# Performance work log

Hardware: AMD Instinct MI355X
Metric: run time of the kernel (lower is better)

## Reference

```python
import jax, jax.numpy as jnp
from jax import lax
import numpy as np

KERNEL_SIZE = 24

def setup_inputs() -> dict:
    key = jax.random.key(0)
    k1, k2, k3, k4 = jax.random.split(key, 4)
    B, C, T = 16, 1024, 3000
    x = jax.random.normal(k1, (B, C, T, 1), dtype=jnp.float32)
    alpha = jax.random.uniform(k2, (C,), dtype=jnp.float32)   # in (0,1): decaying kernels
    beta = jax.random.normal(k3, (C,), dtype=jnp.float32)
    theta = jax.random.uniform(k4, (C,), dtype=jnp.float32)
    return {"x": x, "alpha": alpha, "beta": beta, "theta": theta}

def _cos_approx(x):
    x2 = x * x
    return 1.0 - 0.5 * x2 + (x2 * x2) * (1.0 / 24.0)

def reference(x, alpha, beta, theta):
    B, C, T, _ = x.shape
    K = KERNEL_SIZE
    t_idx = jnp.arange(K, dtype=x.dtype)                      # (K,)
    log_alpha = jnp.log(jnp.clip(alpha, 1e-6))                # (C,)
    decay = jnp.exp(log_alpha[:, None] * t_idx)               # (C,K)
    phase = _cos_approx(theta[:, None] * t_idx)               # (C,K)
    kernel = (beta[:, None] * decay * phase)[:, None, :]      # (C,1,K) depthwise
    # causal depthwise conv1d: left-pad K-1 (torch F.conv1d and lax conv are both correlations)
    y = lax.conv_general_dilated(
        x[..., 0], kernel,
        window_strides=(1,), padding=[(K - 1, 0)],
        dimension_numbers=("NCH", "OIH", "NCH"),
        feature_group_count=C,
    )                                                         # (B,C,T)
    return y[..., None]                                       # (B,C,T,1)
```

## Files before the change

kernel.cpp:

```cpp
#include <hip/hip_runtime.h>


#define KSZ   24
#define T_LEN 3000
#define C_CH  1024
#define B_N   16
#define TPB   256
#define OPT   4
#define TILE  (TPB * OPT)
#define CHK   (T_LEN / 4)
#define PADC  (KSZ / 4)
#define LMAX  (CHK + PADC - 1)
#define PPOS(L) ((L) + ((L) >> 3))
#define LDSN  (PPOS(LMAX) + 1)

typedef float f32x4 __attribute__((ext_vector_type(4)));

__device__ __forceinline__ float cos_approx(float v) {
    float v2 = v * v;
    return 1.0f - 0.5f * v2 + (v2 * v2) * (1.0f / 24.0f);
}

__global__ __launch_bounds__(TPB) void ssm4d_conv(
        const float* __restrict__ x,
        const float* __restrict__ alpha,
        const float* __restrict__ beta,
        const float* __restrict__ theta,
        float* __restrict__ y) {
    const int row   = blockIdx.x;
    const int c     = row & (C_CH - 1);
    const long base = (long)row * T_LEN;
    const int tid   = threadIdx.x;

    __shared__ float ws[KSZ];
    __shared__ f32x4 lds[LDSN];

    const f32x4* xp = (const f32x4*)(x + base);
    const int c0 = tid, c1 = tid + TPB, c2 = tid + 2 * TPB;
    f32x4 a0 = xp[c0];
    f32x4 a1 = xp[c1];
    f32x4 a2 = (c2 < CHK) ? xp[c2] : (f32x4){0.f, 0.f, 0.f, 0.f};

    if (tid < KSZ) {
        const int k = (KSZ - 1) - tid;
        const float a   = fmaxf(alpha[c], 1e-6f);
        const float dec = expf(logf(a) * (float)k);
        ws[tid] = beta[c] * dec * cos_approx(theta[c] * (float)k);
    }
    if (tid < PADC) lds[tid] = (f32x4){0.f, 0.f, 0.f, 0.f};

    lds[PPOS(c0 + PADC)] = a0;
    lds[PPOS(c1 + PADC)] = a1;
    if (c2 < CHK) lds[PPOS(c2 + PADC)] = a2;
    __syncthreads();

    float wr[KSZ];
#pragma unroll
    for (int d = 0; d < KSZ; ++d) wr[d] = ws[d];

#pragma unroll
    for (int s = 0; s < 3; ++s) {
        const int t = s * TILE + tid * OPT;
        if (t < T_LEN) {
            float win[KSZ + OPT];
            const int L0 = s * (TILE / 4) + tid;
#pragma unroll
            for (int q = 0; q < (KSZ + OPT) / 4; ++q) {
                f32x4 v = lds[PPOS(L0 + q)];
                win[4 * q + 0] = v.x; win[4 * q + 1] = v.y;
                win[4 * q + 2] = v.z; win[4 * q + 3] = v.w;
            }
            float acc[OPT];
#pragma unroll
            for (int m = 0; m < OPT; ++m) acc[m] = 0.0f;
#pragma unroll
            for (int d = 0; d < KSZ; ++d) {
#pragma unroll
                for (int m = 0; m < OPT; ++m)
                    acc[m] = fmaf(wr[d], win[KSZ + m - d], acc[m]);
            }
            *(float4*)(y + base + t) = make_float4(acc[0], acc[1], acc[2], acc[3]);
        }
    }
}

extern "C" void kernel_launch(void* const* d_in, const int* in_sizes, int n_in,
                              void* d_out, int out_size, void* d_ws, size_t ws_size,
                              hipStream_t stream) {
    const float* x     = (const float*)d_in[0];
    const float* alpha = (const float*)d_in[1];
    const float* beta  = (const float*)d_in[2];
    const float* theta = (const float*)d_in[3];
    float* y = (float*)d_out;

    ssm4d_conv<<<B_N * C_CH, TPB, 0, stream>>>(x, alpha, beta, theta, y);
}
```

Before: 328.1 us.

## Process four rows per block with double-buffered async global-to-LDS loads

Each block now handles four consecutive rows instead of one. The next row's input is prefetched straight into a second LDS buffer with global_load_lds while the current row is convolved, and its filter taps are computed in the same step. This aims to hide global load latency and spread per-block launch and setup cost over more work. In exchange it drops the padded LDS indexing, which may bring back bank conflicts, and it relies on the barrier waiting for the async LDS loads to finish.

After: 337.4 us. +2.8%, slower.

```diff
diff --git a/kernel.cpp b/kernel.cpp
--- a/kernel.cpp
+++ b/kernel.cpp
@@ -10,9 +10,9 @@
 #define TILE  (TPB * OPT)
 #define CHK   (T_LEN / 4)
 #define PADC  (KSZ / 4)
-#define LMAX  (CHK + PADC - 1)
-#define PPOS(L) ((L) + ((L) >> 3))
-#define LDSN  (PPOS(LMAX) + 1)
+#define NCHK  (CHK + PADC)
+#define RPB   4
+#define NBLK  ((B_N * C_CH) / RPB)
 
 typedef float f32x4 __attribute__((ext_vector_type(4)));
 
@@ -21,66 +21,96 @@
     return 1.0f - 0.5f * v2 + (v2 * v2) * (1.0f / 24.0f);
 }
 
+__device__ __forceinline__ void gload16(const float* g, float* l) {
+    __builtin_amdgcn_global_load_lds(
+        (const __attribute__((address_space(1))) void*)g,
+        (__attribute__((address_space(3))) void*)l,
+        16, 0, 0);
+}
+
+__device__ __forceinline__ void stage_row(const float* xr, f32x4* buf, int tid) {
+    gload16(xr + tid * 4,             (float*)&buf[PADC + tid]);
+    gload16(xr + (tid + TPB) * 4,     (float*)&buf[PADC + TPB + tid]);
+    if (tid + 2 * TPB < CHK)
+        gload16(xr + (tid + 2 * TPB) * 4, (float*)&buf[PADC + 2 * TPB + tid]);
+}
+
+__device__ __forceinline__ void calc_w(const float* __restrict__ alpha,
+                                       const float* __restrict__ beta,
+                                       const float* __restrict__ theta,
+                                       int row, float* wsrow, int tid) {
+    if (tid < KSZ) {
+        const int c = row & (C_CH - 1);
+        const int k = (KSZ - 1) - tid;
+        const float a = fmaxf(alpha[c], 1e-6f);
+        wsrow[tid] = beta[c] * expf(logf(a) * (float)k)
+                   * cos_approx(theta[c] * (float)k);
+    }
+}
+
 __global__ __launch_bounds__(TPB) void ssm4d_conv(
         const float* __restrict__ x,
         const float* __restrict__ alpha,
         const float* __restrict__ beta,
         const float* __restrict__ theta,
         float* __restrict__ y) {
-    const int row   = blockIdx.x;
-    const int c     = row & (C_CH - 1);
-    const long base = (long)row * T_LEN;
-    const int tid   = threadIdx.x;
+    const int tid  = threadIdx.x;
+    const int row0 = blockIdx.x * RPB;
 
-    __shared__ float ws[KSZ];
-    __shared__ f32x4 lds[LDSN];
+    __shared__ f32x4 buf[2][NCHK];
+    __shared__ float ws[2][KSZ];
 
-    const f32x4* xp = (const f32x4*)(x + base);
-    const int c0 = tid, c1 = tid + TPB, c2 = tid + 2 * TPB;
-    f32x4 a0 = xp[c0];
-    f32x4 a1 = xp[c1];
-    f32x4 a2 = (c2 < CHK) ? xp[c2] : (f32x4){0.f, 0.f, 0.f, 0.f};
+    if (tid < PADC) {
+        buf[0][tid] = (f32x4){0.f, 0.f, 0.f, 0.f};
+        buf[1][tid] = (f32x4){0.f, 0.f, 0.f, 0.f};
+    }
 
-    if (tid < KSZ) {
-        const int k = (KSZ - 1) - tid;
-        const float a   = fmaxf(alpha[c], 1e-6f);
-        const float dec = expf(logf(a) * (float)k);
-        ws[tid] = beta[c] * dec * cos_approx(theta[c] * (float)k);
-    }
-    if (tid < PADC) lds[tid] = (f32x4){0.f, 0.f, 0.f, 0.f};
-
-    lds[PPOS(c0 + PADC)] = a0;
-    lds[PPOS(c1 + PADC)] = a1;
-    if (c2 < CHK) lds[PPOS(c2 + PADC)] = a2;
+    stage_row(x + (long)row0 * T_LEN, buf[0], tid);
+    calc_w(alpha, beta, theta, row0, ws[0], tid);
     __syncthreads();
 
-    float wr[KSZ];
+    int cur = 0;
+#pragma unroll 1
+    for (int r = 0; r < RPB; ++r) {
+        const int nxt = cur ^ 1;
+
+        if (r + 1 < RPB) {
+            stage_row(x + (long)(row0 + r + 1) * T_LEN, buf[nxt], tid);
+            calc_w(alpha, beta, theta, row0 + r + 1, ws[nxt], tid);
+        }
+
+        float wr[KSZ];
 #pragma unroll
-    for (int d = 0; d < KSZ; ++d) wr[d] = ws[d];
+        for (int d = 0; d < KSZ; ++d) wr[d] = ws[cur][d];
 
+        float* yr = y + (long)(row0 + r) * T_LEN;
 #pragma unroll
-    for (int s = 0; s < 3; ++s) {
-        const int t = s * TILE + tid * OPT;
-        if (t < T_LEN) {
-            float win[KSZ + OPT];
-            const int L0 = s * (TILE / 4) + tid;
+        for (int s = 0; s < 3; ++s) {
+            const int t = s * TILE + tid * OPT;
+            if (t < T_LEN) {
+                const int L0 = s * (TILE / 4) + tid;
+                float win[KSZ + OPT];
 #pragma unroll
-            for (int q = 0; q < (KSZ + OPT) / 4; ++q) {
-                f32x4 v = lds[PPOS(L0 + q)];
-                win[4 * q + 0] = v.x; win[4 * q + 1] = v.y;
-                win[4 * q + 2] = v.z; win[4 * q + 3] = v.w;
+                for (int q = 0; q < (KSZ + OPT) / 4; ++q) {
+                    f32x4 v = buf[cur][L0 + q];
+                    win[4 * q + 0] = v.x; win[4 * q + 1] = v.y;
+                    win[4 * q + 2] = v.z; win[4 * q + 3] = v.w;
+                }
+                float acc[OPT];
+#pragma unroll
+                for (int m = 0; m < OPT; ++m) acc[m] = 0.0f;
+#pragma unroll
+                for (int d = 0; d < KSZ; ++d) {
+#pragma unroll
+                    for (int m = 0; m < OPT; ++m)
+                        acc[m] = fmaf(wr[d], win[KSZ + m - d], acc[m]);
+                }
+                *(float4*)(yr + t) = make_float4(acc[0], acc[1], acc[2], acc[3]);
             }
-            float acc[OPT];
-#pragma unroll
-            for (int m = 0; m < OPT; ++m) acc[m] = 0.0f;
-#pragma unroll
-            for (int d = 0; d < KSZ; ++d) {
-#pragma unroll
-                for (int m = 0; m < OPT; ++m)
-                    acc[m] = fmaf(wr[d], win[KSZ + m - d], acc[m]);
-            }
-            *(float4*)(y + base + t) = make_float4(acc[0], acc[1], acc[2], acc[3]);
         }
+
+        __syncthreads();
+        cur = nxt;
     }
 }
 
@@ -93,5 +123,5 @@
     const float* theta = (const float*)d_in[3];
     float* y = (float*)d_out;
 
-    ssm4d_conv<<<B_N * C_CH, TPB, 0, stream>>>(x, alpha, beta, theta, y);
+    ssm4d_conv<<<NBLK, TPB, 0, stream>>>(x, alpha, beta, theta, y);
 }
```

## Load rows directly to LDS and compute 12 outputs per thread

Applied to the files above, without the earlier changes.

Global loads now go straight into LDS through the global_load_lds builtin, bypassing VGPRs, and the padded LDS indexing is removed. Each thread now computes 12 contiguous outputs instead of three passes of 4. Only 250 of 256 threads are active, which cuts the redundant window loads per output, and launch bounds now request 4 blocks per CU. The costs are LDS bank conflicts from the stride-3 f32x4 reads without padding and higher register pressure.

After: 336.6 us. 1.03x slower.

```diff
diff --git a/kernel.cpp b/kernel.cpp
--- a/kernel.cpp
+++ b/kernel.cpp
@@ -6,13 +6,12 @@
 #define C_CH  1024
 #define B_N   16
 #define TPB   256
-#define OPT   4
-#define TILE  (TPB * OPT)
+#define OPT   12
+#define ACT   (T_LEN / OPT)
 #define CHK   (T_LEN / 4)
 #define PADC  (KSZ / 4)
-#define LMAX  (CHK + PADC - 1)
-#define PPOS(L) ((L) + ((L) >> 3))
-#define LDSN  (PPOS(LMAX) + 1)
+#define NCHK  (CHK + PADC)
+#define WIN   (KSZ + OPT)
 
 typedef float f32x4 __attribute__((ext_vector_type(4)));
 
@@ -21,7 +20,14 @@
     return 1.0f - 0.5f * v2 + (v2 * v2) * (1.0f / 24.0f);
 }
 
-__global__ __launch_bounds__(TPB) void ssm4d_conv(
+__device__ __forceinline__ void gload16(const float* g, float* l) {
+    __builtin_amdgcn_global_load_lds(
+        (const __attribute__((address_space(1))) void*)g,
+        (__attribute__((address_space(3))) void*)l,
+        16, 0, 0);
+}
+
+__global__ __launch_bounds__(TPB, 4) void ssm4d_conv(
         const float* __restrict__ x,
         const float* __restrict__ alpha,
         const float* __restrict__ beta,
@@ -32,55 +38,54 @@
     const long base = (long)row * T_LEN;
     const int tid   = threadIdx.x;
 
+    __shared__ f32x4 buf[NCHK];
     __shared__ float ws[KSZ];
-    __shared__ f32x4 lds[LDSN];
 
-    const f32x4* xp = (const f32x4*)(x + base);
-    const int c0 = tid, c1 = tid + TPB, c2 = tid + 2 * TPB;
-    f32x4 a0 = xp[c0];
-    f32x4 a1 = xp[c1];
-    f32x4 a2 = (c2 < CHK) ? xp[c2] : (f32x4){0.f, 0.f, 0.f, 0.f};
+    const float* xr = x + base;
+    gload16(xr + tid * 4,             (float*)&buf[PADC + tid]);
+    gload16(xr + (tid + TPB) * 4,     (float*)&buf[PADC + TPB + tid]);
+    if (tid + 2 * TPB < CHK)
+        gload16(xr + (tid + 2 * TPB) * 4, (float*)&buf[PADC + 2 * TPB + tid]);
 
     if (tid < KSZ) {
         const int k = (KSZ - 1) - tid;
-        const float a   = fmaxf(alpha[c], 1e-6f);
-        const float dec = expf(logf(a) * (float)k);
-        ws[tid] = beta[c] * dec * cos_approx(theta[c] * (float)k);
+        const float a = fmaxf(alpha[c], 1e-6f);
+        ws[tid] = beta[c] * expf(logf(a) * (float)k)
+                * cos_approx(theta[c] * (float)k);
     }
-    if (tid < PADC) lds[tid] = (f32x4){0.f, 0.f, 0.f, 0.f};
+    if (tid < PADC) buf[tid] = (f32x4){0.f, 0.f, 0.f, 0.f};
 
-    lds[PPOS(c0 + PADC)] = a0;
-    lds[PPOS(c1 + PADC)] = a1;
-    if (c2 < CHK) lds[PPOS(c2 + PADC)] = a2;
     __syncthreads();
 
-    float wr[KSZ];
+    if (tid < ACT) {
+        float wr[KSZ];
 #pragma unroll
-    for (int d = 0; d < KSZ; ++d) wr[d] = ws[d];
+        for (int d = 0; d < KSZ; ++d) wr[d] = ws[d];
 
+        float win[WIN];
+        const f32x4* wp = &buf[3 * tid];
 #pragma unroll
-    for (int s = 0; s < 3; ++s) {
-        const int t = s * TILE + tid * OPT;
-        if (t < T_LEN) {
-            float win[KSZ + OPT];
-            const int L0 = s * (TILE / 4) + tid;
+        for (int q = 0; q < WIN / 4; ++q) {
+            f32x4 v = wp[q];
+            win[4 * q + 0] = v.x; win[4 * q + 1] = v.y;
+            win[4 * q + 2] = v.z; win[4 * q + 3] = v.w;
+        }
+
+        float acc[OPT];
 #pragma unroll
-            for (int q = 0; q < (KSZ + OPT) / 4; ++q) {
-                f32x4 v = lds[PPOS(L0 + q)];
-                win[4 * q + 0] = v.x; win[4 * q + 1] = v.y;
-                win[4 * q + 2] = v.z; win[4 * q + 3] = v.w;
-            }
-            float acc[OPT];
+        for (int m = 0; m < OPT; ++m) acc[m] = 0.0f;
 #pragma unroll
-            for (int m = 0; m < OPT; ++m) acc[m] = 0.0f;
+        for (int d = 0; d < KSZ; ++d) {
 #pragma unroll
-            for (int d = 0; d < KSZ; ++d) {
-#pragma unroll
-                for (int m = 0; m < OPT; ++m)
-                    acc[m] = fmaf(wr[d], win[KSZ + m - d], acc[m]);
-            }
-            *(float4*)(y + base + t) = make_float4(acc[0], acc[1], acc[2], acc[3]);
+            for (int m = 0; m < OPT; ++m)
+                acc[m] = fmaf(wr[d], win[KSZ + m - d], acc[m]);
         }
+
+        const int t = tid * OPT;
+        float* yr = y + base + t;
+        *(float4*)(yr + 0) = make_float4(acc[0], acc[1], acc[2],  acc[3]);
+        *(float4*)(yr + 4) = make_float4(acc[4], acc[5], acc[6],  acc[7]);
+        *(float4*)(yr + 8) = make_float4(acc[8], acc[9], acc[10], acc[11]);
     }
 }
 
```
